# Kernel tuning notes

Hardware: AMD Instinct MI355X
Metric: run time of the kernel (lower is better)

Reference implementation:

```python
import jax, jax.numpy as jnp
import numpy as np

M = 16                      # multiplicity of each irrep block
INV3 = 1.0 / np.sqrt(3.0)   # w3j(1,1,0) component-normalized
INV2 = 1.0 / np.sqrt(2.0)   # w3j(1,1,1) component-normalized
A0 = 1.0 / np.sqrt(2.0 * M) # fan-in norm for 0e outputs (2 paths x mul 16)
A1 = 1.0 / np.sqrt(3.0 * M) # fan-in norm for 1o outputs (3 paths x mul 16)


def setup_inputs() -> dict:
    E, N, ED, HID = 100000, 10000, 32, 128
    WNUM = 2 * M * (2 * M) + 3 * M * M  # 1792 per-edge TP weights
    ks = jax.random.split(jax.random.key(0), 10)
    return {
        "dst": jax.random.randint(ks[0], (E,), 0, N),
        "x_src": jax.random.normal(ks[1], (E, 4 * M), jnp.float32),   # 16x0e+16x1o
        "x_dst": jax.random.normal(ks[2], (N, 4 * M), jnp.float32),
        "sh": jax.random.normal(ks[3], (E, 4), jnp.float32),          # 1x0e+1x1o
        "edge_attr": jax.random.normal(ks[4], (E, ED), jnp.float32),
        "We1": jax.random.normal(ks[5], (ED, HID), jnp.float32) / np.sqrt(ED),
        "be1": jnp.zeros((HID,), jnp.float32),
        "We2": jax.random.normal(ks[6], (HID, WNUM), jnp.float32) / np.sqrt(HID),
        "be2": jnp.zeros((WNUM,), jnp.float32),
        "Wr0": jax.random.normal(ks[7], (M, 2 * M), jnp.float32),     # 16x0e -> 32x0e
        "Wr1": jax.random.normal(ks[8], (M, M), jnp.float32),         # 16x1o -> 16x1o
    }


def _forward(dst, x_src, x_dst, sh, edge_attr, We1, be1, We2, be2, Wr0, Wr1):
    E = x_src.shape[0]
    N = x_dst.shape[0]
    o0 = 2 * M  # 32x0e tp output (scalars + gates)

    # edge MLP -> per-edge tensor-product weights [E, 1792]
    w = jax.nn.relu(edge_attr @ We1 + be1) @ We2 + be2
    i = 0
    w_ss = w[:, i:i + M * o0].reshape(E, M, o0); i += M * o0   # 0e x 0e -> 0e
    w_vv0 = w[:, i:i + M * o0].reshape(E, M, o0); i += M * o0  # 1o x 1o -> 0e
    w_sv = w[:, i:i + M * M].reshape(E, M, M); i += M * M      # 0e x 1o -> 1o
    w_vs = w[:, i:i + M * M].reshape(E, M, M); i += M * M      # 1o x 0e -> 1o
    w_vv1 = w[:, i:i + M * M].reshape(E, M, M)                 # 1o x 1o -> 1o

    s1 = x_src[:, :M]                       # [E, 16]
    v1 = x_src[:, M:].reshape(E, M, 3)      # [E, 16, 3]
    s2 = sh[:, 0]                           # [E]
    v2 = sh[:, 1:4]                         # [E, 3]

    # fully-connected tensor product with per-edge weights
    out0 = A0 * (jnp.einsum('em,emo->eo', s1 * s2[:, None], w_ss)
                 + INV3 * jnp.einsum('emc,ec,emo->eo', v1, v2, w_vv0))  # [E, 32]
    cross = jnp.cross(v1, v2[:, None, :])   # [E, 16, 3]
    out1 = A1 * (jnp.einsum('em,ec,emo->eoc', s1, v2, w_sv)
                 + jnp.einsum('emc,e,emo->eoc', v1, s2, w_vs)
                 + INV2 * jnp.einsum('emc,emo->eoc', cross, w_vv1))     # [E, 16, 3]
    msg = jnp.concatenate([out0, out1.reshape(E, -1)], axis=1)          # [E, 80]

    # scatter-mean over destination nodes
    ssum = jax.ops.segment_sum(msg, dst, num_segments=N)
    cnt = jax.ops.segment_sum(jnp.ones((E,), msg.dtype), dst, num_segments=N)
    msg = ssum / jnp.maximum(cnt, 1.0)[:, None]                          # [N, 80]

    # residual equivariant linear on x_dst
    sd = x_dst[:, :M]
    vd = x_dst[:, M:].reshape(N, M, 3)
    res0 = (sd @ Wr0) / np.sqrt(M)                                       # [N, 32]
    res1 = jnp.einsum('nmc,mo->noc', vd, Wr1) / np.sqrt(M)               # [N, 16, 3]
    msg = msg + jnp.concatenate([res0, res1.reshape(N, -1)], axis=1)

    # gate nonlinearity: relu(scalars), sigmoid(gates) * gated vectors
    scalars = jax.nn.relu(msg[:, :M])
    gates = jax.nn.sigmoid(msg[:, M:2 * M])
    gated = msg[:, 2 * M:].reshape(N, M, 3) * gates[:, :, None]
    return jnp.concatenate([scalars, gated.reshape(N, -1)], axis=1)      # [N, 64]


def reference(dst, x_src, x_dst, sh, edge_attr, We1, be1, We2, be2, Wr0, Wr1):
    return _forward(dst, x_src, x_dst, sh, edge_attr, We1, be1, We2, be2, Wr0, Wr1)
```

## Files before the change

### kernel.cpp

```cpp
#include <hip/hip_runtime.h>
#include <math.h>

#define WNUM 1792
#define HID 128

#define INV3C 0.5773502691896258f
#define INV2C 0.7071067811865476f
#define A0C   0.17677669529663687f
#define A1C   0.14433756729740643f
#define MAXDEG 64

typedef short bf8 __attribute__((ext_vector_type(8)));
typedef _Float16 f16x8 __attribute__((ext_vector_type(8)));
typedef _Float16 f16x4 __attribute__((ext_vector_type(4)));
typedef float f32x4 __attribute__((ext_vector_type(4)));

__device__ inline unsigned short f2bf(float f) {
  union { float f; unsigned u; } v; v.f = f;
  unsigned r = v.u + 0x7FFFu + ((v.u >> 16) & 1u);
  return (unsigned short)(r >> 16);
}
__device__ inline float bf2f(unsigned short h) {
  union { unsigned u; float f; } v; v.u = ((unsigned)h) << 16;
  return v.f;
}
__device__ inline float wscale(int t) {
  if (t < 32) return A0C;
  if (t < 64) return A0C * INV3C;
  if (t < 96) return A1C;
  return A1C * INV2C;
}

__global__ __launch_bounds__(256) void prep_kernel(
    const float* __restrict__ We1, const float* __restrict__ We2,
    const float* __restrict__ be2,
    unsigned short* __restrict__ we1x, _Float16* __restrict__ we2h,
    float* __restrict__ be2p, int* __restrict__ cntp, int N)
{
  int i = blockIdx.x * 256 + threadIdx.x;
  if (i < 28672) {
    int t = i >> 8, c = (i >> 6) & 3, lane = i & 63;
    int quad = lane >> 4, l15 = lane & 15;
    int col = t * 16 + l15;
    float sc = wscale(t);
    f16x8 v;
    #pragma unroll
    for (int j = 0; j < 8; ++j) {
      int k = c * 32 + quad * 8 + j;
      v[j] = (_Float16)(We2[(size_t)k * WNUM + col] * sc);
    }
    *(f16x8*)(we2h + (size_t)t * 2048 + c * 512 + lane * 8) = v;
  } else if (i < 29184) {
    int q = i - 28672;
    int c1 = q >> 6, lane = q & 63;
    int quad = lane >> 4, l15 = lane & 15;
    int col = c1 * 16 + l15;
    bf8 hh, ll;
    #pragma unroll
    for (int j = 0; j < 8; ++j) {
      int k = quad * 8 + j;
      float v = We1[k * HID + col];
      unsigned short hi = f2bf(v);
      hh[j] = (short)hi;
      ll[j] = (short)f2bf(v - bf2f(hi));
    }
    *(bf8*)(we1x + c1 * 1024 + lane * 8) = hh;
    *(bf8*)(we1x + c1 * 1024 + 512 + lane * 8) = ll;
  } else if (i < 30976) {
    int q = i - 29184;
    int t = q >> 4, l16 = q & 15;
    be2p[(t >> 1) * 32 + l16 * 2 + (t & 1)] = be2[q] * wscale(t);
  } else if (i < 30976 + N) {
    cntp[i - 30976] = 0;
  }
}

__device__ inline void chains2(const f16x8* a0, const f16x8* a1,
    f16x8 b0, f16x8 b1, f16x8 b2, f16x8 b3,
    f16x8 b4, f16x8 b5, f16x8 b6, f16x8 b7,
    float2 bias, f32x4* wa, f32x4* wb)
{
  f32x4 ca0 = {bias.x, bias.x, bias.x, bias.x};
  f32x4 cb0 = {bias.y, bias.y, bias.y, bias.y};
  f32x4 ca1 = ca0, cb1 = cb0;
  ca0 = __builtin_amdgcn_mfma_f32_16x16x32_f16(a0[0], b0, ca0, 0, 0, 0);
  cb0 = __builtin_amdgcn_mfma_f32_16x16x32_f16(a0[0], b4, cb0, 0, 0, 0);
  ca1 = __builtin_amdgcn_mfma_f32_16x16x32_f16(a1[0], b0, ca1, 0, 0, 0);
  cb1 = __builtin_amdgcn_mfma_f32_16x16x32_f16(a1[0], b4, cb1, 0, 0, 0);
  ca0 = __builtin_amdgcn_mfma_f32_16x16x32_f16(a0[1], b1, ca0, 0, 0, 0);
  cb0 = __builtin_amdgcn_mfma_f32_16x16x32_f16(a0[1], b5, cb0, 0, 0, 0);
  ca1 = __builtin_amdgcn_mfma_f32_16x16x32_f16(a1[1], b1, ca1, 0, 0, 0);
  cb1 = __builtin_amdgcn_mfma_f32_16x16x32_f16(a1[1], b5, cb1, 0, 0, 0);
  ca0 = __builtin_amdgcn_mfma_f32_16x16x32_f16(a0[2], b2, ca0, 0, 0, 0);
  cb0 = __builtin_amdgcn_mfma_f32_16x16x32_f16(a0[2], b6, cb0, 0, 0, 0);
  ca1 = __builtin_amdgcn_mfma_f32_16x16x32_f16(a1[2], b2, ca1, 0, 0, 0);
  cb1 = __builtin_amdgcn_mfma_f32_16x16x32_f16(a1[2], b6, cb1, 0, 0, 0);
  ca0 = __builtin_amdgcn_mfma_f32_16x16x32_f16(a0[3], b3, ca0, 0, 0, 0);
  cb0 = __builtin_amdgcn_mfma_f32_16x16x32_f16(a0[3], b7, cb0, 0, 0, 0);
  ca1 = __builtin_amdgcn_mfma_f32_16x16x32_f16(a1[3], b3, ca1, 0, 0, 0);
  cb1 = __builtin_amdgcn_mfma_f32_16x16x32_f16(a1[3], b7, cb1, 0, 0, 0);
  wa[0] = ca0; wb[0] = cb0; wa[1] = ca1; wb[1] = cb1;
}

__device__ inline void pair_mm(const _Float16* bL, const float* bp, int p,
                               const f16x8 (&af)[2][4], f32x4* wa, f32x4* wb)
{
  f16x8 b0 = *(const f16x8*)(bL);
  f16x8 b1 = *(const f16x8*)(bL + 512);
  f16x8 b2 = *(const f16x8*)(bL + 1024);
  f16x8 b3 = *(const f16x8*)(bL + 1536);
  f16x8 b4 = *(const f16x8*)(bL + 2048);
  f16x8 b5 = *(const f16x8*)(bL + 2560);
  f16x8 b6 = *(const f16x8*)(bL + 3072);
  f16x8 b7 = *(const f16x8*)(bL + 3584);
  float2 bias2 = *(const float2*)(bp + p * 32);
  chains2(af[0], af[1], b0, b1, b2, b3, b4, b5, b6, b7, bias2, wa, wb);
}

template <bool MSG>
__global__ __launch_bounds__(256, 2) void edge_kernel(
    const float* __restrict__ ea, const float* __restrict__ xsrc,
    const float* __restrict__ sh, const int* __restrict__ dst,
    const float* __restrict__ be1,
    const unsigned short* __restrict__ we1x, const _Float16* __restrict__ we2h,
    const float* __restrict__ be2p,
    float* __restrict__ outp, int* __restrict__ eidx, int* __restrict__ cntp, int E)
{
  const int lane = threadIdx.x & 63;
  const int w    = threadIdx.x >> 6;
  const int quad = lane >> 4;
  const int l16  = lane & 15;
  const int eb   = (blockIdx.x * 4 + w) * 32;

  __shared__ union SMem {
    _Float16 h[4][32][136];
    _Float16 B[4][4096];
  } uS;
  __shared__ _Float16 s1h_s[4][16][32];
  __shared__ _Float16 v1h_s[4][16][3][32];
  __shared__ float4 vq_s[4][32];

  #define STAGE_PAIR(p) { \
    const _Float16* gsrc_ = we2h + (size_t)(p) * 4096; \
    _Float16* ldst_ = &uS.B[(p) & 3][0]; \
    __builtin_amdgcn_global_load_lds( \
      (const __attribute__((address_space(1))) void*)(gsrc_ + (w * 2) * 512 + lane * 8), \
      (__attribute__((address_space(3))) void*)(ldst_ + (w * 2) * 512), 16, 0, 0); \
    __builtin_amdgcn_global_load_lds( \
      (const __attribute__((address_space(1))) void*)(gsrc_ + (w * 2 + 1) * 512 + lane * 8), \
      (__attribute__((address_space(3))) void*)(ldst_ + (w * 2 + 1) * 512), 16, 0, 0); \
  }

  if (lane < 32) {
    int ge = eb + lane;
    if (ge < E) {
      int node = dst[ge];
      int pos = atomicAdd(cntp + node, 1);
      if (MSG) { if (pos < MAXDEG) eidx[node * MAXDEG + pos] = ge; }
    }
  }

  {
    int e2 = lane >> 1, mg = lane & 1;
    int ge = eb + e2;
    if (ge < E) {
      const float* xp = xsrc + (size_t)ge * 64;
      float4 sq0 = *(const float4*)(xp + mg * 8);
      float4 sq1 = *(const float4*)(xp + mg * 8 + 4);
      float s1a[8] = {sq0.x,sq0.y,sq0.z,sq0.w,sq1.x,sq1.y,sq1.z,sq1.w};
      const float* vp = xp + 16 + mg * 24;
      float la[24];
      #pragma unroll
      for (int qv = 0; qv < 6; ++qv) {
        float4 t = *(const float4*)(vp + qv * 4);
        la[qv*4+0] = t.x; la[qv*4+1] = t.y; la[qv*4+2] = t.z; la[qv*4+3] = t.w;
      }
      float4 shq = *(const float4*)(sh + (size_t)ge * 4);
      float s2 = shq.x, v2x = shq.y, v2y = shq.z, v2z = shq.w;
      #pragma unroll
      for (int mi = 0; mi < 8; ++mi) {
        int m = mg * 8 + mi;
        float v1x = la[mi*3], v1y = la[mi*3+1], v1z = la[mi*3+2];
        s1h_s[w][m][e2] = (_Float16)s1a[mi];
        v1h_s[w][m][0][e2] = (_Float16)v1x;
        v1h_s[w][m][1][e2] = (_Float16)v1y;
        v1h_s[w][m][2][e2] = (_Float16)v1z;
      }
      if (mg == 0) vq_s[w][e2] = make_float4(v2x, v2y, v2z, s2);
    } else {
      #pragma unroll
      for (int mi = 0; mi < 8; ++mi) {
        int m = mg * 8 + mi;
        s1h_s[w][m][e2] = (_Float16)0.f;
        v1h_s[w][m][0][e2] = (_Float16)0.f;
        v1h_s[w][m][1][e2] = (_Float16)0.f;
        v1h_s[w][m][2][e2] = (_Float16)0.f;
      }
      if (mg == 0) vq_s[w][e2] = make_float4(0,0,0,0);
    }
  }

  {
    bf8 ah[2], al[2];
    #pragma unroll
    for (int g = 0; g < 2; ++g) {
      int gea = eb + g * 16 + l16; if (gea > E - 1) gea = E - 1;
      const float* ep = ea + (size_t)gea * 32 + quad * 8;
      float4 p0 = *(const float4*)ep;
      float4 p1 = *(const float4*)(ep + 4);
      float pv[8] = {p0.x,p0.y,p0.z,p0.w,p1.x,p1.y,p1.z,p1.w};
      #pragma unroll
      for (int j = 0; j < 8; ++j) {
        unsigned short hi = f2bf(pv[j]);
        ah[g][j] = (short)hi;
        al[g][j] = (short)f2bf(pv[j] - bf2f(hi));
      }
    }
    const unsigned short* wb1 = we1x + lane * 8;
    #pragma unroll 2
    for (int c = 0; c < 8; ++c) {
      bf8 bh = *(const bf8*)(wb1 + c * 1024);
      bf8 bl = *(const bf8*)(wb1 + c * 1024 + 512);
      float bias = be1[c * 16 + l16];
      #pragma unroll
      for (int g = 0; g < 2; ++g) {
        f32x4 hc = {bias, bias, bias, bias};
        hc = __builtin_amdgcn_mfma_f32_16x16x32_bf16(al[g], bh, hc, 0, 0, 0);
        hc = __builtin_amdgcn_mfma_f32_16x16x32_bf16(ah[g], bl, hc, 0, 0, 0);
        hc = __builtin_amdgcn_mfma_f32_16x16x32_bf16(ah[g], bh, hc, 0, 0, 0);
        #pragma unroll
        for (int r = 0; r < 4; ++r)
          uS.h[w][g * 16 + quad * 4 + r][c * 16 + l16] = (_Float16)fmaxf(hc[r], 0.f);
      }
    }
  }
  __syncthreads();

  f16x8 af[2][4];
  #pragma unroll
  for (int g = 0; g < 2; ++g)
    #pragma unroll
    for (int ch = 0; ch < 4; ++ch)
      af[g][ch] = *(const f16x8*)&uS.h[w][g * 16 + l16][ch * 32 + quad * 8];
  __syncthreads();

  STAGE_PAIR(0)
  STAGE_PAIR(1)
  __syncthreads();

  const float* bp = be2p + l16 * 2;
  float m0a[2][4] = {{0,0,0,0},{0,0,0,0}}, m0b[2][4] = {{0,0,0,0},{0,0,0,0}};

  {
    float s2v[2][4];
    #pragma unroll
    for (int g = 0; g < 2; ++g)
      #pragma unroll
      for (int r = 0; r < 4; ++r)
        s2v[g][r] = vq_s[w][g * 16 + quad * 4 + r].w;

    #pragma unroll 1
    for (int i = 0; i < 16; i += 2) {
      STAGE_PAIR(i + 2)
      STAGE_PAIR(i + 3)
      f32x4 wa[2], wb[2];
      pair_mm(&uS.B[i & 3][lane * 8], bp, i, af, wa, wb);
      #pragma unroll
      for (int g = 0; g < 2; ++g) {
        f16x4 fv = *(const f16x4*)&s1h_s[w][i][g * 16 + quad * 4];
        #pragma unroll
        for (int r = 0; r < 4; ++r) {
          float f = (float)fv[r] * s2v[g][r];
          m0a[g][r] = fmaf(wa[g][r], f, m0a[g][r]);
          m0b[g][r] = fmaf(wb[g][r], f, m0b[g][r]);
        }
      }
      pair_mm(&uS.B[(i + 1) & 3][lane * 8], bp, i + 1, af, wa, wb);
      #pragma unroll
      for (int g = 0; g < 2; ++g) {
        f16x4 fv = *(const f16x4*)&s1h_s[w][i + 1][g * 16 + quad * 4];
        #pragma unroll
        for (int r = 0; r < 4; ++r) {
          float f = (float)fv[r] * s2v[g][r];
          m0a[g][r] = fmaf(wa[g][r], f, m0a[g][r]);
          m0b[g][r] = fmaf(wb[g][r], f, m0b[g][r]);
        }
      }
      __syncthreads();
    }
  }

  {
    float v2xv[2][4], v2yv[2][4], v2zv[2][4];
    #pragma unroll
    for (int g = 0; g < 2; ++g)
      #pragma unroll
      for (int r = 0; r < 4; ++r) {
        float4 q = vq_s[w][g * 16 + quad * 4 + r];
        v2xv[g][r] = q.x; v2yv[g][r] = q.y; v2zv[g][r] = q.z;
      }

    #pragma unroll 1
    for (int i = 0; i < 16; i += 2) {
      int pg = 16 + i;
      STAGE_PAIR(pg + 2)
      STAGE_PAIR(pg + 3)
      f32x4 wa[2], wb[2];
      pair_mm(&uS.B[pg & 3][lane * 8], bp, pg, af, wa, wb);
      #pragma unroll
      for (int g = 0; g < 2; ++g) {
        f16x4 xA = *(const f16x4*)&v1h_s[w][i][0][g * 16 + quad * 4];
        f16x4 yA = *(const f16x4*)&v1h_s[w][i][1][g * 16 + quad * 4];
        f16x4 zA = *(const f16x4*)&v1h_s[w][i][2][g * 16 + quad * 4];
        #pragma unroll
        for (int r = 0; r < 4; ++r) {
          float f = fmaf((float)zA[r], v2zv[g][r],
                    fmaf((float)yA[r], v2yv[g][r], (float)xA[r] * v2xv[g][r]));
          m0a[g][r] = fmaf(wa[g][r], f, m0a[g][r]);
          m0b[g][r] = fmaf(wb[g][r], f, m0b[g][r]);
        }
      }
      pair_mm(&uS.B[(pg + 1) & 3][lane * 8], bp, pg + 1, af, wa, wb);
      #pragma unroll
      for (int g = 0; g < 2; ++g) {
        f16x4 xA = *(const f16x4*)&v1h_s[w][i + 1][0][g * 16 + quad * 4];
        f16x4 yA = *(const f16x4*)&v1h_s[w][i + 1][1][g * 16 + quad * 4];
        f16x4 zA = *(const f16x4*)&v1h_s[w][i + 1][2][g * 16 + quad * 4];
        #pragma unroll
        for (int r = 0; r < 4; ++r) {
          float f = fmaf((float)zA[r], v2zv[g][r],
                    fmaf((float)yA[r], v2yv[g][r], (float)xA[r] * v2xv[g][r]));
          m0a[g][r] = fmaf(wa[g][r], f, m0a[g][r]);
          m0b[g][r] = fmaf(wb[g][r], f, m0b[g][r]);
        }
      }
      __syncthreads();
    }
  }

  #pragma unroll
  for (int g = 0; g < 2; ++g)
    #pragma unroll
    for (int r = 0; r < 4; ++r) {
      int ge = eb + g * 16 + quad * 4 + r;
      if (ge < E) {
        if (MSG) {
          float* mp = outp + (size_t)ge * 80;
          mp[l16]      = m0a[g][r];
          mp[16 + l16] = m0b[g][r];
        } else {
          float* ap = outp + (size_t)dst[ge] * 80;
          atomicAdd(ap + l16,      m0a[g][r]);
          atomicAdd(ap + 16 + l16, m0b[g][r]);
        }
      }
    }

  float sg[2][4] = {{0,0,0,0},{0,0,0,0}};
  #pragma unroll 1
  for (int i = 0; i < 8; i += 2) {
    int pg = 32 + i;
    STAGE_PAIR(pg + 2)
    STAGE_PAIR(pg + 3)
    f32x4 wa[2], wb[2];
    pair_mm(&uS.B[pg & 3][lane * 8], bp, pg, af, wa, wb);
    #pragma unroll
    for (int g = 0; g < 2; ++g) {
      f16x4 sA = *(const f16x4*)&s1h_s[w][2*i][g * 16 + quad * 4];
      f16x4 sB = *(const f16x4*)&s1h_s[w][2*i + 1][g * 16 + quad * 4];
      #pragma unroll
      for (int r = 0; r < 4; ++r)
        sg[g][r] = fmaf(wb[g][r], (float)sB[r], fmaf(wa[g][r], (float)sA[r], sg[g][r]));
    }
    pair_mm(&uS.B[(pg + 1) & 3][lane * 8], bp, pg + 1, af, wa, wb);
    #pragma unroll
    for (int g = 0; g < 2; ++g) {
      f16x4 sA = *(const f16x4*)&s1h_s[w][2*i + 2][g * 16 + quad * 4];
      f16x4 sB = *(const f16x4*)&s1h_s[w][2*i + 3][g * 16 + quad * 4];
      #pragma unroll
      for (int r = 0; r < 4; ++r)
        sg[g][r] = fmaf(wb[g][r], (float)sB[r], fmaf(wa[g][r], (float)sA[r], sg[g][r]));
    }
    __syncthreads();
  }
  float4 vq[2][4];
  #pragma unroll
  for (int g = 0; g < 2; ++g)
    #pragma unroll
    for (int r = 0; r < 4; ++r) vq[g][r] = vq_s[w][g * 16 + quad * 4 + r];

  float m1x[2][4], m1y[2][4], m1z[2][4];
  #pragma unroll
  for (int g = 0; g < 2; ++g)
    #pragma unroll
    for (int r = 0; r < 4; ++r) {
      m1x[g][r] = sg[g][r] * vq[g][r].x;
      m1y[g][r] = sg[g][r] * vq[g][r].y;
      m1z[g][r] = sg[g][r] * vq[g][r].z;
    }

  #pragma unroll
  for (int sec = 0; sec < 2; ++sec) {
    float ux[2][4] = {{0,0,0,0},{0,0,0,0}}, uy[2][4] = {{0,0,0,0},{0,0,0,0}},
          uz[2][4] = {{0,0,0,0},{0,0,0,0}};
    int base = 40 + sec * 8;
    #pragma unroll 1
    for (int i = 0; i < 8; i += 2) {
      int pg = base + i;
      if (pg + 2 < 56) STAGE_PAIR(pg + 2)
      if (pg + 3 < 56) STAGE_PAIR(pg + 3)
      f32x4 wa[2], wb[2];
      pair_mm(&uS.B[pg & 3][lane * 8], bp, pg, af, wa, wb);
      #pragma unroll
      for (int g = 0; g < 2; ++g) {
        f16x4 xA = *(const f16x4*)&v1h_s[w][2*i][0][g*16 + quad*4];
        f16x4 xB = *(const f16x4*)&v1h_s[w][2*i+1][0][g*16 + quad*4];
        f16x4 yA = *(const f16x4*)&v1h_s[w][2*i][1][g*16 + quad*4];
        f16x4 yB = *(const f16x4*)&v1h_s[w][2*i+1][1][g*16 + quad*4];
        f16x4 zA = *(const f16x4*)&v1h_s[w][2*i][2][g*16 + quad*4];
        f16x4 zB = *(const f16x4*)&v1h_s[w][2*i+1][2][g*16 + quad*4];
        #pragma unroll
        for (int r = 0; r < 4; ++r) {
          ux[g][r] = fmaf(wb[g][r], (float)xB[r], fmaf(wa[g][r], (float)xA[r], ux[g][r]));
          uy[g][r] = fmaf(wb[g][r], (float)yB[r], fmaf(wa[g][r], (float)yA[r], uy[g][r]));
          uz[g][r] = fmaf(wb[g][r], (float)zB[r], fmaf(wa[g][r], (float)zA[r], uz[g][r]));
        }
      }
      pair_mm(&uS.B[(pg + 1) & 3][lane * 8], bp, pg + 1, af, wa, wb);
      #pragma unroll
      for (int g = 0; g < 2; ++g) {
        f16x4 xA = *(const f16x4*)&v1h_s[w][2*i+2][0][g*16 + quad*4];
        f16x4 xB = *(const f16x4*)&v1h_s[w][2*i+3][0][g*16 + quad*4];
        f16x4 yA = *(const f16x4*)&v1h_s[w][2*i+2][1][g*16 + quad*4];
        f16x4 yB = *(const f16x4*)&v1h_s[w][2*i+3][1][g*16 + quad*4];
        f16x4 zA = *(const f16x4*)&v1h_s[w][2*i+2][2][g*16 + quad*4];
        f16x4 zB = *(const f16x4*)&v1h_s[w][2*i+3][2][g*16 + quad*4];
        #pragma unroll
        for (int r = 0; r < 4; ++r) {
          ux[g][r] = fmaf(wb[g][r], (float)xB[r], fmaf(wa[g][r], (float)xA[r], ux[g][r]));
          uy[g][r] = fmaf(wb[g][r], (float)yB[r], fmaf(wa[g][r], (float)yA[r], uy[g][r]));
          uz[g][r] = fmaf(wb[g][r], (float)zB[r], fmaf(wa[g][r], (float)zA[r], uz[g][r]));
        }
      }
      __syncthreads();
    }
    if (sec == 0) {
      #pragma unroll
      for (int g = 0; g < 2; ++g)
        #pragma unroll
        for (int r = 0; r < 4; ++r) {
          m1x[g][r] = fmaf(vq[g][r].w, ux[g][r], m1x[g][r]);
          m1y[g][r] = fmaf(vq[g][r].w, uy[g][r], m1y[g][r]);
          m1z[g][r] = fmaf(vq[g][r].w, uz[g][r], m1z[g][r]);
        }
    } else {
      #pragma unroll
      for (int g = 0; g < 2; ++g)
        #pragma unroll
        for (int r = 0; r < 4; ++r) {
          m1x[g][r] = fmaf(uy[g][r], vq[g][r].z, m1x[g][r]);
          m1x[g][r] = fmaf(-uz[g][r], vq[g][r].y, m1x[g][r]);
          m1y[g][r] = fmaf(uz[g][r], vq[g][r].x, m1y[g][r]);
          m1y[g][r] = fmaf(-ux[g][r], vq[g][r].z, m1y[g][r]);
          m1z[g][r] = fmaf(ux[g][r], vq[g][r].y, m1z[g][r]);
          m1z[g][r] = fmaf(-uy[g][r], vq[g][r].x, m1z[g][r]);
        }
    }
  }

  #pragma unroll
  for (int g = 0; g < 2; ++g)
    #pragma unroll
    for (int r = 0; r < 4; ++r) {
      int ge = eb + g * 16 + quad * 4 + r;
      if (ge < E) {
        if (MSG) {
          float* mp = outp + (size_t)ge * 80;
          mp[32 + l16*3 + 0] = m1x[g][r];
          mp[32 + l16*3 + 1] = m1y[g][r];
          mp[32 + l16*3 + 2] = m1z[g][r];
        } else {
          float* ap = outp + (size_t)dst[ge] * 80;
          atomicAdd(ap + 32 + l16*3 + 0, m1x[g][r]);
          atomicAdd(ap + 32 + l16*3 + 1, m1y[g][r]);
          atomicAdd(ap + 32 + l16*3 + 2, m1z[g][r]);
        }
      }
    }
  #undef STAGE_PAIR
}

__global__ __launch_bounds__(128) void node_gather_kernel(
    const float* __restrict__ msg, const int* __restrict__ eidx,
    const int* __restrict__ cntp,
    const float* __restrict__ xdst, const float* __restrict__ Wr0,
    const float* __restrict__ Wr1, float* __restrict__ out, int N)
{
  int n = blockIdx.x;
  if (n >= N) return;
  int j = threadIdx.x;
  int c0 = cntp[n];
  int deg = c0 < MAXDEG ? c0 : MAXDEG;
  float inv = 1.0f / fmaxf((float)c0, 1.0f);
  __shared__ float s_sum[80];
  if (j < 80) {
    float s = 0.f;
    const int* ep = eidx + (size_t)n * MAXDEG;
    int i = 0;
    for (; i + 1 < deg; i += 2) {
      int e0 = ep[i], e1 = ep[i + 1];
      s += msg[(size_t)e0 * 80 + j] + msg[(size_t)e1 * 80 + j];
    }
    if (i < deg) s += msg[(size_t)ep[i] * 80 + j];
    s_sum[j] = s * inv;
  }
  __syncthreads();
  if (j >= 64) return;
  const float* xd = xdst + (size_t)n * 64;
  float* op = out + (size_t)n * 64;
  if (j < 16) {
    float s = 0.f;
    #pragma unroll
    for (int m = 0; m < 16; ++m) s = fmaf(xd[m], Wr0[m * 32 + j], s);
    op[j] = fmaxf(s_sum[j] + 0.25f * s, 0.f);
  } else {
    int jj = j - 16;
    int o = (jj * 86) >> 8;
    int c = jj - o * 3;
    float tg = 0.f, v = 0.f;
    #pragma unroll
    for (int m = 0; m < 16; ++m) {
      tg = fmaf(xd[m], Wr0[m * 32 + 16 + o], tg);
      v  = fmaf(xd[16 + m * 3 + c], Wr1[m * 16 + o], v);
    }
    float g = 1.0f / (1.0f + expf(-(s_sum[16 + o] + 0.25f * tg)));
    op[16 + jj] = (s_sum[32 + jj] + 0.25f * v) * g;
  }
}

__global__ __launch_bounds__(256) void node_kernel(
    const float* __restrict__ accn, const int* __restrict__ cntp,
    const float* __restrict__ xdst, const float* __restrict__ Wr0,
    const float* __restrict__ Wr1, float* __restrict__ out, int N)
{
  int idx = blockIdx.x * 256 + threadIdx.x;
  int n = idx >> 6, j = idx & 63;
  if (n >= N) return;
  float inv = 1.0f / fmaxf((float)cntp[n], 1.0f);
  const float* ap = accn + (size_t)n * 80;
  const float* xd = xdst + (size_t)n * 64;
  float* op = out + (size_t)n * 64;
  if (j < 16) {
    float s = 0.f;
    #pragma unroll
    for (int m = 0; m < 16; ++m) s = fmaf(xd[m], Wr0[m * 32 + j], s);
    op[j] = fmaxf(ap[j] * inv + 0.25f * s, 0.f);
  } else {
    int jj = j - 16;
    int o = (jj * 86) >> 8;
    int c = jj - o * 3;
    float tg = 0.f, v = 0.f;
    #pragma unroll
    for (int m = 0; m < 16; ++m) {
      tg = fmaf(xd[m], Wr0[m * 32 + 16 + o], tg);
      v  = fmaf(xd[16 + m * 3 + c], Wr1[m * 16 + o], v);
    }
    float g = 1.0f / (1.0f + expf(-(ap[16 + o] * inv + 0.25f * tg)));
    op[16 + jj] = (ap[32 + jj] * inv + 0.25f * v) * g;
  }
}

extern "C" void kernel_launch(void* const* d_in, const int* in_sizes, int n_in,
                              void* d_out, int out_size, void* d_ws, size_t ws_size,
                              hipStream_t stream)
{
  const int*   dst  = (const int*)d_in[0];
  const float* xsrc = (const float*)d_in[1];
  const float* xdst = (const float*)d_in[2];
  const float* sh   = (const float*)d_in[3];
  const float* ea   = (const float*)d_in[4];
  const float* We1  = (const float*)d_in[5];
  const float* be1  = (const float*)d_in[6];
  const float* We2  = (const float*)d_in[7];
  const float* be2  = (const float*)d_in[8];
  const float* Wr0  = (const float*)d_in[9];
  const float* Wr1  = (const float*)d_in[10];
  const int E = in_sizes[0];
  const int N = in_sizes[2] / 64;

  char* ws = (char*)d_ws;
  _Float16* we2h = (_Float16*)ws;
  unsigned short* we1x = (unsigned short*)(ws + 458752);
  float* be2p = (float*)(ws + 475136);
  int*   cntp = (int*)(ws + 482560);
  size_t off = 482560 + (size_t)N * 4;
  off = (off + 15) & ~(size_t)15;

  size_t need_msg = off + (size_t)N * MAXDEG * 4 + (size_t)E * 80 * 4;
  bool use_msg = (ws_size >= need_msg);

  prep_kernel<<<(30976 + N + 255) / 256, 256, 0, stream>>>(We1, We2, be2,
      we1x, we2h, be2p, cntp, N);

  if (use_msg) {
    int* eidx = (int*)(ws + off);
    float* msg = (float*)(ws + off + (size_t)N * MAXDEG * 4);
    edge_kernel<true><<<(E + 127) / 128, 256, 0, stream>>>(ea, xsrc, sh, dst, be1,
        we1x, we2h, be2p, msg, eidx, cntp, E);
    node_gather_kernel<<<N, 128, 0, stream>>>(msg, eidx, cntp, xdst, Wr0, Wr1,
        (float*)d_out, N);
  } else {
    float* accn = (float*)(ws + off);
    hipMemsetAsync(accn, 0, (size_t)N * 320, stream);
    edge_kernel<false><<<(E + 127) / 128, 256, 0, stream>>>(ea, xsrc, sh, dst, be1,
        we1x, we2h, be2p, accn, (int*)nullptr, cntp, E);
    node_kernel<<<((size_t)N * 64 + 255) / 256, 256, 0, stream>>>(accn, cntp,
        xdst, Wr0, Wr1, (float*)d_out, N);
  }
}
```

Baseline: 201.7 us.

## Use 512-thread edge blocks and process hidden layer in 16-edge halves

Doubles the edge-kernel block to 8 waves (256 edges per block), so each staged pair of We2 weights in LDS is shared by twice as many waves, and each wave now issues one global_load_lds per pair instead of two. The first MLP layer is restructured to handle the two 16-edge groups one after another through a smaller per-wave LDS buffer, loading the A fragments into registers right after each group with an explicit LDS wait. This shrinks the hidden-activation LDS footprint and lowers live registers so 512 threads fit. The risk is register pressure under launch_bounds(512,2), and the larger LDS footprint for 8 waves may limit how many blocks fit per CU.

After: 206.4 us. 2.3% more time.

```diff
diff --git a/kernel.cpp b/kernel.cpp
--- a/kernel.cpp
+++ b/kernel.cpp
@@ -118,7 +118,7 @@
 }
 
 template <bool MSG>
-__global__ __launch_bounds__(256, 2) void edge_kernel(
+__global__ __launch_bounds__(512, 2) void edge_kernel(
     const float* __restrict__ ea, const float* __restrict__ xsrc,
     const float* __restrict__ sh, const int* __restrict__ dst,
     const float* __restrict__ be1,
@@ -130,25 +130,22 @@
   const int w    = threadIdx.x >> 6;
   const int quad = lane >> 4;
   const int l16  = lane & 15;
-  const int eb   = (blockIdx.x * 4 + w) * 32;
+  const int eb   = (blockIdx.x * 8 + w) * 32;
 
   __shared__ union SMem {
-    _Float16 h[4][32][136];
+    _Float16 h[8][16][136];
     _Float16 B[4][4096];
   } uS;
-  __shared__ _Float16 s1h_s[4][16][32];
-  __shared__ _Float16 v1h_s[4][16][3][32];
-  __shared__ float4 vq_s[4][32];
+  __shared__ _Float16 s1h_s[8][16][32];
+  __shared__ _Float16 v1h_s[8][16][3][32];
+  __shared__ float4 vq_s[8][32];
 
   #define STAGE_PAIR(p) { \
     const _Float16* gsrc_ = we2h + (size_t)(p) * 4096; \
     _Float16* ldst_ = &uS.B[(p) & 3][0]; \
     __builtin_amdgcn_global_load_lds( \
-      (const __attribute__((address_space(1))) void*)(gsrc_ + (w * 2) * 512 + lane * 8), \
-      (__attribute__((address_space(3))) void*)(ldst_ + (w * 2) * 512), 16, 0, 0); \
-    __builtin_amdgcn_global_load_lds( \
-      (const __attribute__((address_space(1))) void*)(gsrc_ + (w * 2 + 1) * 512 + lane * 8), \
-      (__attribute__((address_space(3))) void*)(ldst_ + (w * 2 + 1) * 512), 16, 0, 0); \
+      (const __attribute__((address_space(1))) void*)(gsrc_ + w * 512 + lane * 8), \
+      (__attribute__((address_space(3))) void*)(ldst_ + w * 512), 16, 0, 0); \
   }
 
   if (lane < 32) {
@@ -200,48 +197,45 @@
     }
   }
 
+  f16x8 af[2][4];
   {
-    bf8 ah[2], al[2];
+    const unsigned short* wb1 = we1x + lane * 8;
     #pragma unroll
     for (int g = 0; g < 2; ++g) {
-      int gea = eb + g * 16 + l16; if (gea > E - 1) gea = E - 1;
-      const float* ep = ea + (size_t)gea * 32 + quad * 8;
-      float4 p0 = *(const float4*)ep;
-      float4 p1 = *(const float4*)(ep + 4);
-      float pv[8] = {p0.x,p0.y,p0.z,p0.w,p1.x,p1.y,p1.z,p1.w};
-      #pragma unroll
-      for (int j = 0; j < 8; ++j) {
-        unsigned short hi = f2bf(pv[j]);
-        ah[g][j] = (short)hi;
-        al[g][j] = (short)f2bf(pv[j] - bf2f(hi));
-      }
-    }
-    const unsigned short* wb1 = we1x + lane * 8;
-    #pragma unroll 2
-    for (int c = 0; c < 8; ++c) {
-      bf8 bh = *(const bf8*)(wb1 + c * 1024);
-      bf8 bl = *(const bf8*)(wb1 + c * 1024 + 512);
-      float bias = be1[c * 16 + l16];
-      #pragma unroll
-      for (int g = 0; g < 2; ++g) {
+      bf8 ah, al;
+      {
+        int gea = eb + g * 16 + l16; if (gea > E - 1) gea = E - 1;
+        const float* ep = ea + (size_t)gea * 32 + quad * 8;
+        float4 p0 = *(const float4*)ep;
+        float4 p1 = *(const float4*)(ep + 4);
+        float pv[8] = {p0.x,p0.y,p0.z,p0.w,p1.x,p1.y,p1.z,p1.w};
+        #pragma unroll
+        for (int j = 0; j < 8; ++j) {
+          unsigned short hi = f2bf(pv[j]);
+          ah[j] = (short)hi;
+          al[j] = (short)f2bf(pv[j] - bf2f(hi));
+        }
+      }
+      #pragma unroll 2
+      for (int c = 0; c < 8; ++c) {
+        bf8 bh = *(const bf8*)(wb1 + c * 1024);
+        bf8 bl = *(const bf8*)(wb1 + c * 1024 + 512);
+        float bias = be1[c * 16 + l16];
         f32x4 hc = {bias, bias, bias, bias};
-        hc = __builtin_amdgcn_mfma_f32_16x16x32_bf16(al[g], bh, hc, 0, 0, 0);
-        hc = __builtin_amdgcn_mfma_f32_16x16x32_bf16(ah[g], bl, hc, 0, 0, 0);
-        hc = __builtin_amdgcn_mfma_f32_16x16x32_bf16(ah[g], bh, hc, 0, 0, 0);
+        hc = __builtin_amdgcn_mfma_f32_16x16x32_bf16(al, bh, hc, 0, 0, 0);
+        hc = __builtin_amdgcn_mfma_f32_16x16x32_bf16(ah, bl, hc, 0, 0, 0);
+        hc = __builtin_amdgcn_mfma_f32_16x16x32_bf16(ah, bh, hc, 0, 0, 0);
         #pragma unroll
         for (int r = 0; r < 4; ++r)
-          uS.h[w][g * 16 + quad * 4 + r][c * 16 + l16] = (_Float16)fmaxf(hc[r], 0.f);
-      }
-    }
-  }
-  __syncthreads();
-
-  f16x8 af[2][4];
-  #pragma unroll
-  for (int g = 0; g < 2; ++g)
-    #pragma unroll
-    for (int ch = 0; ch < 4; ++ch)
-      af[g][ch] = *(const f16x8*)&uS.h[w][g * 16 + l16][ch * 32 + quad * 8];
+          uS.h[w][quad * 4 + r][c * 16 + l16] = (_Float16)fmaxf(hc[r], 0.f);
+      }
+      #pragma unroll
+      for (int ch = 0; ch < 4; ++ch)
+        af[g][ch] = *(const f16x8*)&uS.h[w][l16][ch * 32 + quad * 8];
+      asm volatile("s_waitcnt lgkmcnt(0)" ::: "memory");
+      __builtin_amdgcn_sched_barrier(0);
+    }
+  }
   __syncthreads();
 
   STAGE_PAIR(0)
@@ -605,14 +599,14 @@
   if (use_msg) {
     int* eidx = (int*)(ws + off);
     float* msg = (float*)(ws + off + (size_t)N * MAXDEG * 4);
-    edge_kernel<true><<<(E + 127) / 128, 256, 0, stream>>>(ea, xsrc, sh, dst, be1,
+    edge_kernel<true><<<(E + 255) / 256, 512, 0, stream>>>(ea, xsrc, sh, dst, be1,
         we1x, we2h, be2p, msg, eidx, cntp, E);
     node_gather_kernel<<<N, 128, 0, stream>>>(msg, eidx, cntp, xdst, Wr0, Wr1,
         (float*)d_out, N);
   } else {
     float* accn = (float*)(ws + off);
     hipMemsetAsync(accn, 0, (size_t)N * 320, stream);
-    edge_kernel<false><<<(E + 127) / 128, 256, 0, stream>>>(ea, xsrc, sh, dst, be1,
+    edge_kernel<false><<<(E + 255) / 256, 512, 0, stream>>>(ea, xsrc, sh, dst, be1,
         we1x, we2h, be2p, accn, (int*)nullptr, cntp, E);
     node_kernel<<<((size_t)N * 64 + 255) / 256, 256, 0, stream>>>(accn, cntp,
         xdst, Wr0, Wr1, (float*)d_out, N);
```
